# Kernel tuning notes

Hardware: AMD Instinct MI355X
Metric: run time of the kernel (lower is better)

## Reference

```python
import jax, jax.numpy as jnp
import numpy as np
import math

B, QL, KL, D = 8, 2048, 2048, 1024


def setup_inputs() -> dict:
    key = jax.random.key(0)
    ks = jax.random.split(key, 9)
    s = 1.0 / math.sqrt(D)
    return {
        "q_embd": jax.random.normal(ks[0], (B, QL, D), jnp.float32),
        "k_embd": jax.random.normal(ks[1], (B, KL, D), jnp.float32),
        "v_embd": jax.random.normal(ks[2], (B, KL, D), jnp.float32),
        "Wq": jax.random.normal(ks[3], (D, D), jnp.float32) * s,
        "bq": jax.random.normal(ks[4], (D,), jnp.float32) * s,
        "Wk": jax.random.normal(ks[5], (D, D), jnp.float32) * s,
        "bk": jax.random.normal(ks[6], (D,), jnp.float32) * s,
        "Wv": jax.random.normal(ks[7], (D, D), jnp.float32) * s,
        "bv": jax.random.normal(ks[8], (D,), jnp.float32) * s,
    }


def reference(q_embd, k_embd, v_embd, Wq, bq, Wk, bk, Wv, bv):
    # Linear projections (torch Linear: x @ W^T + b); head_size==1 so
    # the permute/view multi-head reshuffle is an identity.
    q = jnp.einsum("bsd,hd->bsh", q_embd, Wq) + bq  # [B,QL,D]
    k = jnp.einsum("bsd,hd->bsh", k_embd, Wk) + bk  # [B,KL,D]
    v = jnp.einsum("bsd,hd->bsh", v_embd, Wv) + bv  # [B,KL,D]
    # scaled_dot score: [B,QL,KL]
    scale = 1.0 / jnp.sqrt(jnp.asarray(q.shape[-1], q.dtype))
    score = jnp.einsum("bqd,bkd->bqk", q, k) * scale
    attn = jax.nn.softmax(score, axis=-1)
    out = jnp.einsum("bqk,bkd->bqd", attn, v)  # [B,QL,D]
    return out
```

## Files before the change

kernel.cpp:

```cpp
#include <hip/hip_runtime.h>
#include <hip/hip_bf16.h>

typedef float f32x4 __attribute__((ext_vector_type(4)));
typedef __bf16 bf16x8 __attribute__((ext_vector_type(8)));
typedef unsigned short u16x4 __attribute__((ext_vector_type(4)));

__device__ __forceinline__ unsigned short f2bf(float f) {
  unsigned u = __builtin_bit_cast(unsigned, f);
  u += 0x7FFFu + ((u >> 16) & 1u);
  return (unsigned short)(u >> 16);
}
__device__ __forceinline__ float bf2f(unsigned short h) {
  unsigned u = ((unsigned)h) << 16;
  return __builtin_bit_cast(float, u);
}

__device__ __forceinline__ void gload_lds16(const void* g, void* l) {
  __builtin_amdgcn_global_load_lds(
      (const __attribute__((address_space(1))) void*)g,
      (__attribute__((address_space(3))) void*)l, 16, 0, 0);
}

constexpr int BM = 256, BN = 256, BK = 64;

#define BAR() __builtin_amdgcn_s_barrier()
#define VMW(N) asm volatile("s_waitcnt vmcnt(" #N ")" ::: "memory")
#define PRIO(x) __builtin_amdgcn_s_setprio(x)

#define MM(a_, b_, c_)                                                        \
  c_ = __builtin_amdgcn_mfma_f32_16x16x32_bf16(                               \
      __builtin_bit_cast(bf16x8, a_), __builtin_bit_cast(bf16x8, b_), c_, 0, 0, 0)

template <int OUT_MODE, bool HAS_BIAS>
__global__ __launch_bounds__(512, 2) void gemm256(
    const unsigned short* __restrict__ A, const unsigned short* __restrict__ B,
    const float* __restrict__ bias, float scale, void* __restrict__ Cv,
    int N, int K, long sA, long sB, long sC, int gx, int gy) {
  __shared__ char sm[131072];

  const int nwg = gridDim.x;
  int id = blockIdx.x;
  id = (id & 7) * (nwg >> 3) + (id >> 3);
  const int bx = id % gx;
  const int by = (id / gx) % gy;
  const int bz = id / (gx * gy);

  const int t = threadIdx.x;
  const int lane = t & 63;
  const int w = t >> 6;
  const int wm = w >> 2;
  const int wn = w & 3;

  const int rowBase = by * BM;
  const int colBase = bx * BN;
  const unsigned short* Ab = A + sA * bz;
  const unsigned short* Bb = B + sB * bz;
  const int NT = K >> 6;

  const int srl = lane >> 3;
  const int schunk = (lane & 7) ^ srl;

#define STAGE_A(tt, h, d)                                                     \
  do {                                                                        \
    int _kt = (tt); if (_kt > NT - 1) _kt = NT - 1;                           \
    const int _k0 = _kt << 6;                                                 \
    _Pragma("unroll") for (int _j = 0; _j < 2; ++_j) {                        \
      const int _r = (w + 8 * _j) * 8 + srl;                                  \
      gload_lds16(Ab + (size_t)(rowBase + (h) * 128 + _r) * K + _k0 + schunk * 8, \
                  sm + (d) * 32768 + (h) * 16384 + (w + 8 * _j) * 1024);      \
    }                                                                         \
  } while (0)
#define STAGE_B(tt, h, d)                                                     \
  do {                                                                        \
    int _kt = (tt); if (_kt > NT - 1) _kt = NT - 1;                           \
    const int _k0 = _kt << 6;                                                 \
    _Pragma("unroll") for (int _j = 0; _j < 2; ++_j) {                        \
      const int _r = (w + 8 * _j) * 8 + srl;                                  \
      gload_lds16(Bb + (size_t)(colBase + (h) * 128 + _r) * K + _k0 + schunk * 8, \
                  sm + 65536 + (d) * 32768 + (h) * 16384 + (w + 8 * _j) * 1024); \
    }                                                                         \
  } while (0)

  const int lr = lane & 15;
  const int g0 = lane >> 4;
  const int sw0 = (g0 ^ (lr & 7)) << 4;
  const int sw1 = ((g0 + 4) ^ (lr & 7)) << 4;
  const int aBase = wm * 8192 + lr * 128;
  const int bBase = 65536 + wn * 4096 + lr * 128;

  uint4 Ar[4][2], Br0[2][2], Br1[2][2];
  f32x4 acc[8][4];
#pragma unroll
  for (int m = 0; m < 8; ++m)
#pragma unroll
    for (int n = 0; n < 4; ++n) acc[m][n] = (f32x4){0.f, 0.f, 0.f, 0.f};

#define READ_A(d, mh)                                                         \
  do {                                                                        \
    _Pragma("unroll") for (int f = 0; f < 4; ++f) {                           \
      Ar[f][0] = *(const uint4*)(sm + (d) * 32768 + (mh) * 16384 + aBase + f * 2048 + sw0); \
      Ar[f][1] = *(const uint4*)(sm + (d) * 32768 + (mh) * 16384 + aBase + f * 2048 + sw1); \
    }                                                                         \
  } while (0)
#define READ_B0(d)                                                            \
  do {                                                                        \
    _Pragma("unroll") for (int f = 0; f < 2; ++f) {                           \
      Br0[f][0] = *(const uint4*)(sm + (d) * 32768 + bBase + f * 2048 + sw0); \
      Br0[f][1] = *(const uint4*)(sm + (d) * 32768 + bBase + f * 2048 + sw1); \
    }                                                                         \
  } while (0)
#define READ_B1(d)                                                            \
  do {                                                                        \
    _Pragma("unroll") for (int f = 0; f < 2; ++f) {                           \
      Br1[f][0] = *(const uint4*)(sm + (d) * 32768 + 16384 + bBase + f * 2048 + sw0); \
      Br1[f][1] = *(const uint4*)(sm + (d) * 32768 + 16384 + bBase + f * 2048 + sw1); \
    }                                                                         \
  } while (0)

#define MFMA_Q(Bset, mh, nh)                                                  \
  do {                                                                        \
    _Pragma("unroll") for (int kk = 0; kk < 2; ++kk)                          \
        _Pragma("unroll") for (int mf = 0; mf < 4; ++mf)                      \
            _Pragma("unroll") for (int nf = 0; nf < 2; ++nf)                  \
                MM(Ar[mf][kk], Bset[nf][kk], acc[(mh) * 4 + mf][(nh) * 2 + nf]); \
  } while (0)

#define TILE2(t_, d_)                                                         \
  do {                                                                        \
     READ_B0(d_); READ_B1(d_); READ_A(d_, 0);                       \
    STAGE_A((t_) + 1, 1, (d_) ^ 1);                                           \
    BAR();                                                                    \
    PRIO(1); MFMA_Q(Br0, 0, 0); MFMA_Q(Br1, 0, 1); PRIO(0);                   \
    BAR();                                                                    \
     READ_A(d_, 1);                                                 \
    STAGE_A((t_) + 2, 0, d_); STAGE_B((t_) + 2, 0, d_); STAGE_B((t_) + 2, 1, d_); \
    BAR();                                                                    \
    PRIO(1); MFMA_Q(Br1, 1, 1); MFMA_Q(Br0, 1, 0); PRIO(0);                   \
    VMW(6);                                                                   \
    BAR();                                                                    \
  } while (0)

  STAGE_A(0, 0, 0); STAGE_B(0, 0, 0); STAGE_B(0, 1, 0); STAGE_A(0, 1, 0);
  STAGE_A(1, 0, 1); STAGE_B(1, 0, 1); STAGE_B(1, 1, 1);
  VMW(6);
  BAR();

  for (int i = 0; i < (NT >> 1); ++i) {
    TILE2(2 * i, 0);
    TILE2(2 * i + 1, 1);
  }
  VMW(0);

#pragma unroll
  for (int n = 0; n < 4; ++n) {
    const int col = colBase + (n >> 1) * 128 + wn * 32 + (n & 1) * 16 + lr;
    float bvv = 0.f;
    if constexpr (HAS_BIAS) bvv = bias[col];
#pragma unroll
    for (int m = 0; m < 8; ++m) {
      const int row0 = rowBase + (m >> 2) * 128 + wm * 64 + (m & 3) * 16 + g0 * 4;
      f32x4 v = acc[m][n];
      if constexpr (OUT_MODE == 0) {
        unsigned short* C = (unsigned short*)Cv + sC * bz;
#pragma unroll
        for (int r = 0; r < 4; ++r)
          C[(size_t)(row0 + r) * N + col] = f2bf(v[r] * scale + bvv);
      } else if constexpr (OUT_MODE == 1) {
        unsigned short* C = (unsigned short*)Cv;
        const int b = row0 >> 11, s = row0 & 2047;
        u16x4 pk;
#pragma unroll
        for (int r = 0; r < 4; ++r) pk[r] = f2bf(v[r] * scale + bvv);
        *(u16x4*)&C[((size_t)b * N + col) * 2048 + s] = pk;
      } else {
        float* C = (float*)Cv + sC * bz;
#pragma unroll
        for (int r = 0; r < 4; ++r)
          C[(size_t)(row0 + r) * N + col] = v[r] * scale + bvv;
      }
    }
  }
}

__global__ __launch_bounds__(256) void f32_to_bf16(
    const float* __restrict__ in, unsigned short* __restrict__ out, int n8) {
  int i = blockIdx.x * 256 + threadIdx.x;
  const int stride = gridDim.x * 256;
  for (; i < n8; i += stride) {
    float4 a = ((const float4*)in)[2 * i];
    float4 b = ((const float4*)in)[2 * i + 1];
    unsigned short h[8];
    h[0] = f2bf(a.x); h[1] = f2bf(a.y); h[2] = f2bf(a.z); h[3] = f2bf(a.w);
    h[4] = f2bf(b.x); h[5] = f2bf(b.y); h[6] = f2bf(b.z); h[7] = f2bf(b.w);
    ((uint4*)out)[i] = *(uint4*)h;
  }
}

__global__ __launch_bounds__(256) void softmax_inplace(unsigned short* __restrict__ S) {
  const size_t row = blockIdx.x;
  unsigned short* p = S + row * 2048;
  const int t = threadIdx.x;
  const int lane = t & 63, wid = t >> 6;

  uint4 x = ((const uint4*)p)[t];
  unsigned short* hs = (unsigned short*)&x;
  float f[8];
#pragma unroll
  for (int j = 0; j < 8; ++j) f[j] = bf2f(hs[j]);

  float mx = f[0];
#pragma unroll
  for (int j = 1; j < 8; ++j) mx = fmaxf(mx, f[j]);
#pragma unroll
  for (int d = 1; d < 64; d <<= 1) mx = fmaxf(mx, __shfl_xor(mx, d));
  __shared__ float redm[4];
  if (lane == 0) redm[wid] = mx;
  __syncthreads();
  mx = fmaxf(fmaxf(redm[0], redm[1]), fmaxf(redm[2], redm[3]));

  float e[8], s = 0.f;
#pragma unroll
  for (int j = 0; j < 8; ++j) {
    e[j] = __expf(f[j] - mx);
    s += e[j];
  }
#pragma unroll
  for (int d = 1; d < 64; d <<= 1) s += __shfl_xor(s, d);
  __shared__ float reds[4];
  if (lane == 0) reds[wid] = s;
  __syncthreads();
  s = reds[0] + reds[1] + reds[2] + reds[3];
  const float inv = 1.f / s;

#pragma unroll
  for (int j = 0; j < 8; ++j) hs[j] = f2bf(e[j] * inv);
  ((uint4*)p)[t] = x;
}

extern "C" void kernel_launch(void* const* d_in, const int* in_sizes, int n_in,
                              void* d_out, int out_size, void* d_ws, size_t ws_size,
                              hipStream_t stream) {
  const float* q_embd = (const float*)d_in[0];
  const float* k_embd = (const float*)d_in[1];
  const float* v_embd = (const float*)d_in[2];
  const float* Wq = (const float*)d_in[3];
  const float* bq = (const float*)d_in[4];
  const float* Wk = (const float*)d_in[5];
  const float* bk = (const float*)d_in[6];
  const float* Wv = (const float*)d_in[7];
  const float* bv = (const float*)d_in[8];

  constexpr int B = 8, QL = 2048, KL = 2048, D = 1024;
  constexpr size_t NE = (size_t)B * QL * D;

  unsigned short* qb = (unsigned short*)d_ws;
  unsigned short* kb = qb + NE;
  unsigned short* vT = kb + NE;
  unsigned short* Sb = vT + NE;
  unsigned short* Xe = Sb;
  unsigned short* Wb = Sb + NE;

  dim3 blk256(256), blk512(512);
  const dim3 gconvE(2048), gconvW(512);
  const dim3 gproj(4 * 64);

  f32_to_bf16<<<gconvE, blk256, 0, stream>>>(q_embd, Xe, (int)(NE / 8));
  f32_to_bf16<<<gconvW, blk256, 0, stream>>>(Wq, Wb, D * D / 8);
  gemm256<0, true><<<gproj, blk512, 0, stream>>>(Xe, Wb, bq, 1.0f, qb, D, D,
                                                 0L, 0L, 0L, 4, 64);
  f32_to_bf16<<<gconvE, blk256, 0, stream>>>(k_embd, Xe, (int)(NE / 8));
  f32_to_bf16<<<gconvW, blk256, 0, stream>>>(Wk, Wb, D * D / 8);
  gemm256<0, true><<<gproj, blk512, 0, stream>>>(Xe, Wb, bk, 1.0f, kb, D, D,
                                                 0L, 0L, 0L, 4, 64);
  f32_to_bf16<<<gconvE, blk256, 0, stream>>>(v_embd, Xe, (int)(NE / 8));
  f32_to_bf16<<<gconvW, blk256, 0, stream>>>(Wv, Wb, D * D / 8);
  gemm256<1, true><<<gproj, blk512, 0, stream>>>(Xe, Wb, bv, 1.0f, vT, D, D,
                                                 0L, 0L, 0L, 4, 64);

  gemm256<0, false><<<dim3(512), blk512, 0, stream>>>(
      qb, kb, nullptr, 0.03125f, Sb, KL, D, (long)QL * D, (long)KL * D,
      (long)QL * KL, 8, 8);

  softmax_inplace<<<dim3(B * QL), blk256, 0, stream>>>(Sb);

  gemm256<2, false><<<dim3(256), blk512, 0, stream>>>(
      Sb, vT, nullptr, 1.0f, d_out, D, KL, (long)QL * KL, (long)D * KL,
      (long)QL * D, 4, 8);
}
```

Before: 371.8 us.

## Replace 256x256 GEMM with simpler 128x128 double-buffered GEMM and merge conversions

Swaps the 256x256-tile, 8-wave GEMM and its interleaved half-tile pipeline for a 128x128-tile, 4-wave kernel. The new kernel uses a plain double-buffered loop that stages the next K tile, reads fragments, runs MFMAs and waits on all loads every iteration. It also fuses the embedding and weight fp32-to-bf16 conversions into one launch per projection, and quadruples grid sizes to match. The aim is more workgroups for occupancy and balance and fewer launches, at the cost of lower per-tile data reuse and a full vmcnt(0) wait each iteration instead of partial-overlap waits.

Result: slower. 387.7 us (+4.3%).

```diff
diff --git a/kernel.cpp b/kernel.cpp
--- a/kernel.cpp
+++ b/kernel.cpp
@@ -21,22 +21,20 @@
       (__attribute__((address_space(3))) void*)l, 16, 0, 0);
 }
 
-constexpr int BM = 256, BN = 256, BK = 64;
-
 #define BAR() __builtin_amdgcn_s_barrier()
 #define VMW(N) asm volatile("s_waitcnt vmcnt(" #N ")" ::: "memory")
 #define PRIO(x) __builtin_amdgcn_s_setprio(x)
 
-#define MM(a_, b_, c_)                                                        \
+#define MM16(a_, b_, c_)                                                      \
   c_ = __builtin_amdgcn_mfma_f32_16x16x32_bf16(                               \
       __builtin_bit_cast(bf16x8, a_), __builtin_bit_cast(bf16x8, b_), c_, 0, 0, 0)
 
 template <int OUT_MODE, bool HAS_BIAS>
-__global__ __launch_bounds__(512, 2) void gemm256(
+__global__ __launch_bounds__(256, 2) void gemm128(
     const unsigned short* __restrict__ A, const unsigned short* __restrict__ B,
     const float* __restrict__ bias, float scale, void* __restrict__ Cv,
     int N, int K, long sA, long sB, long sC, int gx, int gy) {
-  __shared__ char sm[131072];
+  __shared__ char sm[65536];
 
   const int nwg = gridDim.x;
   int id = blockIdx.x;
@@ -48,11 +46,11 @@
   const int t = threadIdx.x;
   const int lane = t & 63;
   const int w = t >> 6;
-  const int wm = w >> 2;
-  const int wn = w & 3;
-
-  const int rowBase = by * BM;
-  const int colBase = bx * BN;
+  const int wm = w >> 1;
+  const int wn = w & 1;
+
+  const int rowBase = by * 128;
+  const int colBase = bx * 128;
   const unsigned short* Ab = A + sA * bz;
   const unsigned short* Bb = B + sB * bz;
   const int NT = K >> 6;
@@ -60,24 +58,16 @@
   const int srl = lane >> 3;
   const int schunk = (lane & 7) ^ srl;
 
-#define STAGE_A(tt, h, d)                                                     \
+#define STAGE(tt, d)                                                          \
   do {                                                                        \
     int _kt = (tt); if (_kt > NT - 1) _kt = NT - 1;                           \
     const int _k0 = _kt << 6;                                                 \
-    _Pragma("unroll") for (int _j = 0; _j < 2; ++_j) {                        \
-      const int _r = (w + 8 * _j) * 8 + srl;                                  \
-      gload_lds16(Ab + (size_t)(rowBase + (h) * 128 + _r) * K + _k0 + schunk * 8, \
-                  sm + (d) * 32768 + (h) * 16384 + (w + 8 * _j) * 1024);      \
-    }                                                                         \
-  } while (0)
-#define STAGE_B(tt, h, d)                                                     \
-  do {                                                                        \
-    int _kt = (tt); if (_kt > NT - 1) _kt = NT - 1;                           \
-    const int _k0 = _kt << 6;                                                 \
-    _Pragma("unroll") for (int _j = 0; _j < 2; ++_j) {                        \
-      const int _r = (w + 8 * _j) * 8 + srl;                                  \
-      gload_lds16(Bb + (size_t)(colBase + (h) * 128 + _r) * K + _k0 + schunk * 8, \
-                  sm + 65536 + (d) * 32768 + (h) * 16384 + (w + 8 * _j) * 1024); \
+    _Pragma("unroll") for (int _j = 0; _j < 4; ++_j) {                        \
+      const int _r = w * 32 + _j * 8 + srl;                                   \
+      gload_lds16(Ab + (size_t)(rowBase + _r) * K + _k0 + schunk * 8,         \
+                  sm + (d) * 16384 + (w * 4 + _j) * 1024);                    \
+      gload_lds16(Bb + (size_t)(colBase + _r) * K + _k0 + schunk * 8,         \
+                  sm + 32768 + (d) * 16384 + (w * 4 + _j) * 1024);            \
     }                                                                         \
   } while (0)
 
@@ -86,79 +76,56 @@
   const int sw0 = (g0 ^ (lr & 7)) << 4;
   const int sw1 = ((g0 + 4) ^ (lr & 7)) << 4;
   const int aBase = wm * 8192 + lr * 128;
-  const int bBase = 65536 + wn * 4096 + lr * 128;
-
-  uint4 Ar[4][2], Br0[2][2], Br1[2][2];
-  f32x4 acc[8][4];
-#pragma unroll
-  for (int m = 0; m < 8; ++m)
+  const int bBase = 32768 + wn * 8192 + lr * 128;
+
+  uint4 Ar[4][2], Br[4][2];
+  f32x4 acc[4][4];
+#pragma unroll
+  for (int m = 0; m < 4; ++m)
 #pragma unroll
     for (int n = 0; n < 4; ++n) acc[m][n] = (f32x4){0.f, 0.f, 0.f, 0.f};
 
-#define READ_A(d, mh)                                                         \
+#define READ_FRAGS(d)                                                         \
   do {                                                                        \
     _Pragma("unroll") for (int f = 0; f < 4; ++f) {                           \
-      Ar[f][0] = *(const uint4*)(sm + (d) * 32768 + (mh) * 16384 + aBase + f * 2048 + sw0); \
-      Ar[f][1] = *(const uint4*)(sm + (d) * 32768 + (mh) * 16384 + aBase + f * 2048 + sw1); \
+      Br[f][0] = *(const uint4*)(sm + (d) * 16384 + bBase + f * 2048 + sw0);  \
+      Br[f][1] = *(const uint4*)(sm + (d) * 16384 + bBase + f * 2048 + sw1);  \
+      Ar[f][0] = *(const uint4*)(sm + (d) * 16384 + aBase + f * 2048 + sw0);  \
+      Ar[f][1] = *(const uint4*)(sm + (d) * 16384 + aBase + f * 2048 + sw1);  \
     }                                                                         \
   } while (0)
-#define READ_B0(d)                                                            \
-  do {                                                                        \
-    _Pragma("unroll") for (int f = 0; f < 2; ++f) {                           \
-      Br0[f][0] = *(const uint4*)(sm + (d) * 32768 + bBase + f * 2048 + sw0); \
-      Br0[f][1] = *(const uint4*)(sm + (d) * 32768 + bBase + f * 2048 + sw1); \
-    }                                                                         \
-  } while (0)
-#define READ_B1(d)                                                            \
-  do {                                                                        \
-    _Pragma("unroll") for (int f = 0; f < 2; ++f) {                           \
-      Br1[f][0] = *(const uint4*)(sm + (d) * 32768 + 16384 + bBase + f * 2048 + sw0); \
-      Br1[f][1] = *(const uint4*)(sm + (d) * 32768 + 16384 + bBase + f * 2048 + sw1); \
-    }                                                                         \
-  } while (0)
-
-#define MFMA_Q(Bset, mh, nh)                                                  \
+
+#define MFMA_ALL()                                                            \
   do {                                                                        \
     _Pragma("unroll") for (int kk = 0; kk < 2; ++kk)                          \
         _Pragma("unroll") for (int mf = 0; mf < 4; ++mf)                      \
-            _Pragma("unroll") for (int nf = 0; nf < 2; ++nf)                  \
-                MM(Ar[mf][kk], Bset[nf][kk], acc[(mh) * 4 + mf][(nh) * 2 + nf]); \
+            _Pragma("unroll") for (int nf = 0; nf < 4; ++nf)                  \
+                MM16(Ar[mf][kk], Br[nf][kk], acc[mf][nf]);                    \
   } while (0)
 
-#define TILE2(t_, d_)                                                         \
-  do {                                                                        \
-     READ_B0(d_); READ_B1(d_); READ_A(d_, 0);                       \
-    STAGE_A((t_) + 1, 1, (d_) ^ 1);                                           \
-    BAR();                                                                    \
-    PRIO(1); MFMA_Q(Br0, 0, 0); MFMA_Q(Br1, 0, 1); PRIO(0);                   \
-    BAR();                                                                    \
-     READ_A(d_, 1);                                                 \
-    STAGE_A((t_) + 2, 0, d_); STAGE_B((t_) + 2, 0, d_); STAGE_B((t_) + 2, 1, d_); \
-    BAR();                                                                    \
-    PRIO(1); MFMA_Q(Br1, 1, 1); MFMA_Q(Br0, 1, 0); PRIO(0);                   \
-    VMW(6);                                                                   \
-    BAR();                                                                    \
-  } while (0)
-
-  STAGE_A(0, 0, 0); STAGE_B(0, 0, 0); STAGE_B(0, 1, 0); STAGE_A(0, 1, 0);
-  STAGE_A(1, 0, 1); STAGE_B(1, 0, 1); STAGE_B(1, 1, 1);
-  VMW(6);
+  STAGE(0, 0);
+  VMW(0);
   BAR();
 
-  for (int i = 0; i < (NT >> 1); ++i) {
-    TILE2(2 * i, 0);
-    TILE2(2 * i + 1, 1);
-  }
-  VMW(0);
+  for (int i = 0; i < NT; ++i) {
+    const int d = i & 1;
+    STAGE(i + 1, d ^ 1);
+    READ_FRAGS(d);
+    PRIO(1);
+    MFMA_ALL();
+    PRIO(0);
+    VMW(0);
+    BAR();
+  }
 
 #pragma unroll
   for (int n = 0; n < 4; ++n) {
-    const int col = colBase + (n >> 1) * 128 + wn * 32 + (n & 1) * 16 + lr;
+    const int col = colBase + wn * 64 + n * 16 + lr;
     float bvv = 0.f;
     if constexpr (HAS_BIAS) bvv = bias[col];
 #pragma unroll
-    for (int m = 0; m < 8; ++m) {
-      const int row0 = rowBase + (m >> 2) * 128 + wm * 64 + (m & 3) * 16 + g0 * 4;
+    for (int m = 0; m < 4; ++m) {
+      const int row0 = rowBase + wm * 64 + m * 16 + g0 * 4;
       f32x4 v = acc[m][n];
       if constexpr (OUT_MODE == 0) {
         unsigned short* C = (unsigned short*)Cv + sC * bz;
@@ -182,17 +149,24 @@
   }
 }
 
-__global__ __launch_bounds__(256) void f32_to_bf16(
-    const float* __restrict__ in, unsigned short* __restrict__ out, int n8) {
-  int i = blockIdx.x * 256 + threadIdx.x;
+__global__ __launch_bounds__(256) void conv_pair(
+    const float* __restrict__ e, const float* __restrict__ wt,
+    unsigned short* __restrict__ eo, unsigned short* __restrict__ wo,
+    int ne8, int nw8) {
+  const int tot = ne8 + nw8;
   const int stride = gridDim.x * 256;
-  for (; i < n8; i += stride) {
-    float4 a = ((const float4*)in)[2 * i];
-    float4 b = ((const float4*)in)[2 * i + 1];
+  for (int i = blockIdx.x * 256 + threadIdx.x; i < tot; i += stride) {
+    const float* src;
+    unsigned short* dst;
+    int k;
+    if (i < ne8) { src = e; dst = eo; k = i; }
+    else { src = wt; dst = wo; k = i - ne8; }
+    float4 a = ((const float4*)src)[2 * k];
+    float4 b = ((const float4*)src)[2 * k + 1];
     unsigned short h[8];
     h[0] = f2bf(a.x); h[1] = f2bf(a.y); h[2] = f2bf(a.z); h[3] = f2bf(a.w);
     h[4] = f2bf(b.x); h[5] = f2bf(b.y); h[6] = f2bf(b.z); h[7] = f2bf(b.w);
-    ((uint4*)out)[i] = *(uint4*)h;
+    ((uint4*)dst)[k] = *(uint4*)h;
   }
 }
 
@@ -260,30 +234,28 @@
   unsigned short* Xe = Sb;
   unsigned short* Wb = Sb + NE;
 
-  dim3 blk256(256), blk512(512);
-  const dim3 gconvE(2048), gconvW(512);
-  const dim3 gproj(4 * 64);
-
-  f32_to_bf16<<<gconvE, blk256, 0, stream>>>(q_embd, Xe, (int)(NE / 8));
-  f32_to_bf16<<<gconvW, blk256, 0, stream>>>(Wq, Wb, D * D / 8);
-  gemm256<0, true><<<gproj, blk512, 0, stream>>>(Xe, Wb, bq, 1.0f, qb, D, D,
-                                                 0L, 0L, 0L, 4, 64);
-  f32_to_bf16<<<gconvE, blk256, 0, stream>>>(k_embd, Xe, (int)(NE / 8));
-  f32_to_bf16<<<gconvW, blk256, 0, stream>>>(Wk, Wb, D * D / 8);
-  gemm256<0, true><<<gproj, blk512, 0, stream>>>(Xe, Wb, bk, 1.0f, kb, D, D,
-                                                 0L, 0L, 0L, 4, 64);
-  f32_to_bf16<<<gconvE, blk256, 0, stream>>>(v_embd, Xe, (int)(NE / 8));
-  f32_to_bf16<<<gconvW, blk256, 0, stream>>>(Wv, Wb, D * D / 8);
-  gemm256<1, true><<<gproj, blk512, 0, stream>>>(Xe, Wb, bv, 1.0f, vT, D, D,
-                                                 0L, 0L, 0L, 4, 64);
-
-  gemm256<0, false><<<dim3(512), blk512, 0, stream>>>(
+  dim3 blk256(256);
+  const dim3 gconv(2048);
+  const dim3 gproj(8 * 128);
+  constexpr int NE8 = (int)(NE / 8), NW8 = D * D / 8;
+
+  conv_pair<<<gconv, blk256, 0, stream>>>(q_embd, Wq, Xe, Wb, NE8, NW8);
+  gemm128<0, true><<<gproj, blk256, 0, stream>>>(Xe, Wb, bq, 1.0f, qb, D, D,
+                                                 0L, 0L, 0L, 8, 128);
+  conv_pair<<<gconv, blk256, 0, stream>>>(k_embd, Wk, Xe, Wb, NE8, NW8);
+  gemm128<0, true><<<gproj, blk256, 0, stream>>>(Xe, Wb, bk, 1.0f, kb, D, D,
+                                                 0L, 0L, 0L, 8, 128);
+  conv_pair<<<gconv, blk256, 0, stream>>>(v_embd, Wv, Xe, Wb, NE8, NW8);
+  gemm128<1, true><<<gproj, blk256, 0, stream>>>(Xe, Wb, bv, 1.0f, vT, D, D,
+                                                 0L, 0L, 0L, 8, 128);
+
+  gemm128<0, false><<<dim3(2048), blk256, 0, stream>>>(
       qb, kb, nullptr, 0.03125f, Sb, KL, D, (long)QL * D, (long)KL * D,
-      (long)QL * KL, 8, 8);
+      (long)QL * KL, 16, 16);
 
   softmax_inplace<<<dim3(B * QL), blk256, 0, stream>>>(Sb);
 
-  gemm256<2, false><<<dim3(256), blk512, 0, stream>>>(
+  gemm128<2, false><<<dim3(1024), blk256, 0, stream>>>(
       Sb, vT, nullptr, 1.0f, d_out, D, KL, (long)QL * KL, (long)D * KL,
-      (long)QL * D, 4, 8);
-}
+      (long)QL * D, 8, 16);
+}
```
